# Optimization experiments

Hardware: AMD Instinct MI355X
Metric: run time of the kernel (lower is better)

## Reference

```python
import jax, jax.numpy as jnp
import numpy as np

HEADS = 8
DIM_HEAD = 64
DIM_COOR = 3
SCALE = (DIM_COOR * DIM_HEAD) ** -0.5


def setup_inputs() -> dict:
    key = jax.random.key(0)
    k1, k2, k3 = jax.random.split(key, 3)
    x = jax.random.normal(k1, (2, 2048, 256, 3), dtype=jnp.float32)
    w_qkv = jax.random.normal(k2, (1536, 256), dtype=jnp.float32)
    w_out = jax.random.normal(k3, (256, 512), dtype=jnp.float32)
    return {"x": x, "w_qkv": w_qkv, "w_out": w_out}


def reference(x, w_qkv, w_out):
    b, n, _, c = x.shape
    # VNLinear: contract feature dim, keep coord dim  -> [b, n, 3*h*d, c]
    qkv = jnp.einsum('bnic,oi->bnoc', x, w_qkv)
    q, k, v = jnp.split(qkv, 3, axis=-2)  # each [b, n, h*d, c]

    def to_heads(t):
        return t.reshape(b, n, HEADS, DIM_HEAD, c).transpose(0, 2, 1, 3, 4)  # b h n d c

    q, k, v = map(to_heads, (q, k, v))
    q = q * SCALE
    # scores sum over head-dim AND coordinate-dim
    sim = jnp.einsum('bhidc,bhjdc->bhij', q, k)
    attn = jax.nn.softmax(sim, axis=-1)
    out = jnp.einsum('bhij,bhjdc->bhidc', attn, v)  # coord dim preserved
    out = out.transpose(0, 2, 1, 3, 4).reshape(b, n, HEADS * DIM_HEAD, c)
    return jnp.einsum('bnic,oi->bnoc', out, w_out)
```

## Files before the change

### kernel.cpp

```cpp
#include <hip/hip_runtime.h>
#include <hip/hip_bf16.h>

#define SCALE 0.07216878364870322f
#define LOG2E 1.4426950408889634f

typedef __bf16 bf16x8 __attribute__((ext_vector_type(8)));
typedef float f32x16 __attribute__((ext_vector_type(16)));
typedef float f32x4v __attribute__((ext_vector_type(4)));
typedef unsigned int u32x4 __attribute__((ext_vector_type(4)));
typedef unsigned short u16;

#define MFMA(a, b, c) __builtin_amdgcn_mfma_f32_32x32x16_bf16(a, b, c, 0, 0, 0)
#define MFMA16(a, b, c) __builtin_amdgcn_mfma_f32_16x16x32_bf16(a, b, c, 0, 0, 0)

__device__ __forceinline__ u16 b16(float v) { return __builtin_bit_cast(u16, (__bf16)v); }
__device__ __forceinline__ float fb16(u16 u) {
    unsigned int t = (unsigned int)u << 16;
    return __builtin_bit_cast(float, t);
}
__device__ __forceinline__ unsigned int splitpack(float v) {
    u16 h = b16(v);
    float r = v - fb16(h);
    return (unsigned int)h | ((unsigned int)b16(r) << 16);
}
__device__ __forceinline__ unsigned int pack2(float a, float b) {
    return (unsigned int)b16(a) | ((unsigned int)b16(b) << 16);
}
__device__ __forceinline__ void gload16(const void* g, void* l) {
    __builtin_amdgcn_global_load_lds((const __attribute__((address_space(1))) void*)g,
                                     (__attribute__((address_space(3))) void*)l, 16, 0, 0);
}

__global__ __launch_bounds__(256) void qkv_mfma(const float* __restrict__ x,
                                                const float* __restrict__ wq,
                                                u16* __restrict__ Qhi, u16* __restrict__ Qlo,
                                                u16* __restrict__ Khi, u16* __restrict__ Klo,
                                                u16* __restrict__ Vf) {
    __shared__ unsigned int ldsr[2][32][196];
    const int tid = threadIdx.x;
    const int lane = tid & 63, w = tid >> 6, hf = lane >> 5, l31 = lane & 31;
    const int lq = lane & 15, gq = lane >> 4;
    const int o0 = blockIdx.x * 64;
    const int n0 = blockIdx.y * 128;
    const int b = blockIdx.z;
    const int nw0 = n0 + w * 32;
    const int part = o0 >> 9;
    const int h = (o0 >> 6) & 7;
    const int bh = b * 8 + h;

    const float* xp = x + ((size_t)(b * 2048 + nw0 + l31)) * 768 + hf * 24;
    const float* wp0 = wq + (size_t)(o0 + l31) * 256 + hf * 8;
    const float* wp1 = wp0 + 32 * 256;

    f32x16 acc[3][2] = {};
    #pragma unroll 2
    for (int k0 = 0; k0 < 16; ++k0) {
        float xf[24], wf0[8], wf1[8];
        #pragma unroll
        for (int q = 0; q < 6; ++q) {
            f32x4v t = *(const f32x4v*)(xp + k0 * 48 + q * 4);
            xf[q * 4 + 0] = t[0]; xf[q * 4 + 1] = t[1];
            xf[q * 4 + 2] = t[2]; xf[q * 4 + 3] = t[3];
        }
        {
            f32x4v t0 = *(const f32x4v*)(wp0 + k0 * 16);
            f32x4v t1 = *(const f32x4v*)(wp0 + k0 * 16 + 4);
            f32x4v t2 = *(const f32x4v*)(wp1 + k0 * 16);
            f32x4v t3 = *(const f32x4v*)(wp1 + k0 * 16 + 4);
            #pragma unroll
            for (int e = 0; e < 4; ++e) {
                wf0[e] = t0[e]; wf0[4 + e] = t1[e];
                wf1[e] = t2[e]; wf1[4 + e] = t3[e];
            }
        }
        bf16x8 xh[3], xl[3], wh[2], wl[2];
        #pragma unroll
        for (int c = 0; c < 3; ++c)
            #pragma unroll
            for (int e = 0; e < 8; ++e) {
                float v = xf[e * 3 + c];
                __bf16 hi = (__bf16)v;
                xh[c][e] = hi;
                xl[c][e] = (__bf16)(v - (float)hi);
            }
        #pragma unroll
        for (int e = 0; e < 8; ++e) {
            { float v = wf0[e]; __bf16 hi = (__bf16)v; wh[0][e] = hi; wl[0][e] = (__bf16)(v - (float)hi); }
            { float v = wf1[e]; __bf16 hi = (__bf16)v; wh[1][e] = hi; wl[1][e] = (__bf16)(v - (float)hi); }
        }
        #pragma unroll
        for (int c = 0; c < 3; ++c)
            #pragma unroll
            for (int ot = 0; ot < 2; ++ot) {
                acc[c][ot] = MFMA(xh[c], wh[ot], acc[c][ot]);
                acc[c][ot] = MFMA(xl[c], wh[ot], acc[c][ot]);
                acc[c][ot] = MFMA(xh[c], wl[ot], acc[c][ot]);
            }
    }

    #pragma unroll
    for (int round = 0; round < 2; ++round) {
        __syncthreads();
        if ((w >> 1) == round) {
            unsigned int (*L)[196] = ldsr[w & 1];
            #pragma unroll
            for (int c = 0; c < 3; ++c)
                #pragma unroll
                for (int ot = 0; ot < 2; ++ot)
                    #pragma unroll
                    for (int r = 0; r < 16; ++r) {
                        float v = acc[c][ot][r];
                        if (part == 0) v *= (SCALE * LOG2E);
                        int nn = (r & 3) + 8 * (r >> 2) + 4 * hf;
                        int dcol = 3 * (ot * 32 + l31) + c;
                        L[nn][dcol] = (part == 2) ? (unsigned int)b16(v) : splitpack(v);
                    }
            if (part < 2) {
                const int jt = nw0 >> 6;
                u16* baseH = (part == 0 ? Qhi : Khi);
                u16* baseL = (part == 0 ? Qlo : Klo);
                #pragma unroll
                for (int is = 0; is < 2; ++is)
                    #pragma unroll
                    for (int kc = 0; kc < 6; ++kc) {
                        const unsigned int* p = &L[is * 16 + lq][kc * 32 + gq * 8];
                        u32x4 a = *(const u32x4*)p;
                        u32x4 bq = *(const u32x4*)(p + 4);
                        u32x4 hi = { (a[0] & 0xffffu) | (a[1] << 16), (a[2] & 0xffffu) | (a[3] << 16),
                                     (bq[0] & 0xffffu) | (bq[1] << 16), (bq[2] & 0xffffu) | (bq[3] << 16) };
                        u32x4 lo = { (a[0] >> 16) | (a[1] & 0xffff0000u), (a[2] >> 16) | (a[3] & 0xffff0000u),
                                     (bq[0] >> 16) | (bq[1] & 0xffff0000u), (bq[2] >> 16) | (bq[3] & 0xffff0000u) };
                        size_t off;
                        if (part == 0)
                            off = ((size_t)(bh * 128 + (nw0 >> 4) + is) * 6 + kc) * 512 + lane * 8;
                        else
                            off = ((size_t)(bh * 32 + jt) * 24 + ((((nw0 >> 4) & 3) + is) * 6 + kc)) * 512 + lane * 8;
                        *(u32x4*)(baseH + off) = hi;
                        *(u32x4*)(baseL + off) = lo;
                    }
            } else {
                const int jt = nw0 >> 6, jc = (nw0 >> 5) & 1;
                u16* vp = Vf + ((size_t)(bh * 32 + jt) * 24 + jc) * 512 + lane * 8;
                #pragma unroll
                for (int d = 0; d < 12; ++d) {
                    unsigned int t[8];
                    #pragma unroll
                    for (int e = 0; e < 8; ++e)
                        t[e] = L[gq * 8 + e][d * 16 + lq];
                    u32x4 pk = { (t[0] & 0xffffu) | (t[1] << 16), (t[2] & 0xffffu) | (t[3] << 16),
                                 (t[4] & 0xffffu) | (t[5] << 16), (t[6] & 0xffffu) | (t[7] << 16) };
                    *(u32x4*)(vp + d * 1024) = pk;
                }
            }
        }
    }
}

__global__ __launch_bounds__(512) void attn_mfma(
    const u16* __restrict__ Qhi, const u16* __restrict__ Qlo,
    const u16* __restrict__ Khi, const u16* __restrict__ Klo,
    const u16* __restrict__ Vf, unsigned int* __restrict__ att2) {
    __shared__ __align__(16) u16 lds[2][36864];
    const int tid = threadIdx.x;
    const int lane = tid & 63;
    const int w = tid >> 6;
    const int g = lane >> 4;
    const int i = lane & 15;
    const int id = blockIdx.x;
    const int bh = (id & 7) * 2 + (id >> 7);
    const int itile = (id >> 3) & 15;
    const int i0 = itile * 128 + w * 16;

    bf16x8 qh[6], ql[6];
    {
        size_t qb = ((size_t)(bh * 128 + (i0 >> 4)) * 6) * 512 + (size_t)lane * 8;
        #pragma unroll
        for (int kc = 0; kc < 6; ++kc) {
            qh[kc] = *(const bf16x8*)(Qhi + qb + kc * 512);
            ql[kc] = *(const bf16x8*)(Qlo + qb + kc * 512);
        }
    }

    const char* gK = (const char*)Khi + (size_t)bh * 786432;
    const char* gL = (const char*)Klo + (size_t)bh * 786432;
    const char* gV = (const char*)Vf + (size_t)bh * 786432;
    const int t16 = tid * 16;

    auto stage = [&](int buf, int jt) {
        const size_t jo = (size_t)jt * 24576 + t16;
        char* dst = (char*)&lds[buf][0] + t16;
        #pragma unroll
        for (int s = 0; s < 3; ++s) {
            gload16(gK + jo + s * 8192, dst + s * 8192);
            gload16(gL + jo + s * 8192, dst + 24576 + s * 8192);
            gload16(gV + jo + s * 8192, dst + 49152 + s * 8192);
        }
    };

    stage(0, 0);
    __syncthreads();
    int cur = 0;

    f32x4v o[12] = {};
    float m_run = -1e30f, l_run = 0.f;
    const int sl0 = ((g & 1) << 5) + i;
    const int sl1 = sl0 + 16;
    const bool ghi = (g >> 1) != 0;

    for (int jt = 0; jt < 32; ++jt) {
        if (jt + 1 < 32) stage(cur ^ 1, jt + 1);
        const u16* L = &lds[cur][0];

        f32x4v s4[4] = {};
        #pragma unroll
        for (int kc = 0; kc < 6; ++kc) {
            bf16x8 kh[4], kl[4];
            #pragma unroll
            for (int js = 0; js < 4; ++js) {
                kh[js] = *(const bf16x8*)&L[(unsigned)((js * 6 + kc) * 512) + lane * 8];
                kl[js] = *(const bf16x8*)&L[12288u + (unsigned)((js * 6 + kc) * 512) + lane * 8];
            }
            #pragma unroll
            for (int js = 0; js < 4; ++js) s4[js] = MFMA16(kh[js], qh[kc], s4[js]);
            #pragma unroll
            for (int js = 0; js < 4; ++js) s4[js] = MFMA16(kh[js], ql[kc], s4[js]);
            #pragma unroll
            for (int js = 0; js < 4; ++js) s4[js] = MFMA16(kl[js], qh[kc], s4[js]);
        }

        float pm = -1e30f;
        #pragma unroll
        for (int js = 0; js < 4; ++js)
            #pragma unroll
            for (int r = 0; r < 4; ++r) pm = fmaxf(pm, s4[js][r]);
        pm = fmaxf(pm, __shfl_xor(pm, 16, 64));
        pm = fmaxf(pm, __shfl_xor(pm, 32, 64));
        if (!__all(pm <= m_run + 8.0f)) {
            float mnew = fmaxf(m_run, pm);
            float sc = exp2f(m_run - mnew);
            l_run *= sc;
            #pragma unroll
            for (int d = 0; d < 12; ++d) o[d] = o[d] * sc;
            m_run = mnew;
        }
        float rs = 0.f;
        unsigned int w0[4], w1[4];
        #pragma unroll
        for (int js = 0; js < 4; ++js) {
            float p0 = exp2f(s4[js][0] - m_run), p1 = exp2f(s4[js][1] - m_run);
            float p2 = exp2f(s4[js][2] - m_run), p3 = exp2f(s4[js][3] - m_run);
            rs += (p0 + p1) + (p2 + p3);
            w0[js] = pack2(p0, p1);
            w1[js] = pack2(p2, p3);
        }
        rs += __shfl_xor(rs, 16, 64);
        rs += __shfl_xor(rs, 32, 64);
        l_run += rs;

        #pragma unroll
        for (int c = 0; c < 2; ++c) {
            u32x4 F;
            { unsigned a0 = __shfl((int)w0[2 * c], sl0, 64), a1 = __shfl((int)w0[2 * c + 1], sl0, 64); F[0] = ghi ? a1 : a0; }
            { unsigned a0 = __shfl((int)w1[2 * c], sl0, 64), a1 = __shfl((int)w1[2 * c + 1], sl0, 64); F[1] = ghi ? a1 : a0; }
            { unsigned a0 = __shfl((int)w0[2 * c], sl1, 64), a1 = __shfl((int)w0[2 * c + 1], sl1, 64); F[2] = ghi ? a1 : a0; }
            { unsigned a0 = __shfl((int)w1[2 * c], sl1, 64), a1 = __shfl((int)w1[2 * c + 1], sl1, 64); F[3] = ghi ? a1 : a0; }
            bf16x8 pb = __builtin_bit_cast(bf16x8, F);
            #pragma unroll
            for (int d = 0; d < 12; ++d) {
                bf16x8 vf = *(const bf16x8*)&L[24576u + (unsigned)((d * 2 + c) * 512) + lane * 8];
                o[d] = MFMA16(vf, pb, o[d]);
            }
        }

        if (jt + 1 < 32) {
            __syncthreads();
            cur ^= 1;
        }
    }

    float inv = 1.0f / l_run;
    const int b2 = bh >> 3, hh = bh & 7;
    const int ig = i0 + i;
    const int itq = ig >> 5, i31 = ig & 31;
    #pragma unroll
    for (int d = 0; d < 12; ++d)
        #pragma unroll
        for (int r = 0; r < 4; ++r) {
            int dc = d * 16 + g * 4 + r;
            int dd = dc / 3, cc2 = dc - dd * 3;
            int hd = hh * 64 + dd;
            int ks = hd >> 4, e = hd & 7;
            int ln = i31 | (((hd >> 3) & 1) << 5);
            size_t off = (((size_t)(b2 * 3 + cc2) * 32 + ks) * 64 + itq) * 512 + (size_t)ln * 8 + e;
            att2[off] = splitpack(o[d][r] * inv);
        }
}

__global__ __launch_bounds__(256) void out_mfma(const unsigned int* __restrict__ att2,
                                                const float* __restrict__ wo,
                                                float* __restrict__ out) {
    const int tid = threadIdx.x, lane = tid & 63, w = tid >> 6, hf = lane >> 5, l31 = lane & 31;
    const int o0 = blockIdx.x * 32;
    const int n5 = blockIdx.y * 4 + w;
    const int b = blockIdx.z;
    const float* wp = wo + (size_t)(o0 + l31) * 512 + hf * 8;
    const unsigned int* ap = att2 + ((size_t)(b * 3) * 2048 + n5) * 512 + (size_t)lane * 8;
    f32x16 acc[3] = {};
    #pragma unroll 2
    for (int ks = 0; ks < 32; ++ks) {
        bf16x8 wh, wl;
        {
            f32x4v t0 = *(const f32x4v*)(wp + ks * 16);
            f32x4v t1 = *(const f32x4v*)(wp + ks * 16 + 4);
            #pragma unroll
            for (int e = 0; e < 4; ++e) {
                { float v = t0[e]; __bf16 hi = (__bf16)v; wh[e] = hi; wl[e] = (__bf16)(v - (float)hi); }
                { float v = t1[e]; __bf16 hi = (__bf16)v; wh[4 + e] = hi; wl[4 + e] = (__bf16)(v - (float)hi); }
            }
        }
        #pragma unroll
        for (int c = 0; c < 3; ++c) {
            const unsigned int* pc = ap + (size_t)c * 1048576 + ks * 32768;
            u32x4 a0 = *(const u32x4*)pc;
            u32x4 a1 = *(const u32x4*)(pc + 4);
            union { bf16x8 v; u32x4 u; } H, Lo;
            H.u  = { (a0[0] & 0xffffu) | (a0[1] << 16), (a0[2] & 0xffffu) | (a0[3] << 16),
                     (a1[0] & 0xffffu) | (a1[1] << 16), (a1[2] & 0xffffu) | (a1[3] << 16) };
            Lo.u = { (a0[0] >> 16) | (a0[1] & 0xffff0000u), (a0[2] >> 16) | (a0[3] & 0xffff0000u),
                     (a1[0] >> 16) | (a1[1] & 0xffff0000u), (a1[2] >> 16) | (a1[3] & 0xffff0000u) };
            acc[c] = MFMA(H.v, wh, acc[c]);
            acc[c] = MFMA(Lo.v, wh, acc[c]);
            acc[c] = MFMA(H.v, wl, acc[c]);
        }
    }
    #pragma unroll
    for (int r = 0; r < 16; ++r) {
        int n = (n5 << 5) + (r & 3) + 8 * (r >> 2) + 4 * hf;
        size_t off = ((size_t)(b * 2048 + n) * 256 + o0 + l31) * 3;
        out[off]     = acc[0][r];
        out[off + 1] = acc[1][r];
        out[off + 2] = acc[2][r];
    }
}

extern "C" void kernel_launch(void* const* d_in, const int* in_sizes, int n_in,
                              void* d_out, int out_size, void* d_ws, size_t ws_size,
                              hipStream_t stream) {
    const float* x     = (const float*)d_in[0];
    const float* w_qkv = (const float*)d_in[1];
    const float* w_out = (const float*)d_in[2];
    float* out = (float*)d_out;

    const size_t NB = (size_t)16 * 2048 * 192;
    u16* Qhi = (u16*)d_ws;
    u16* Qlo = Qhi + NB;
    u16* Khi = Qlo + NB;
    u16* Klo = Khi + NB;
    u16* Vf  = Klo + NB;
    unsigned int* att2 = (unsigned int*)(Vf + NB);

    qkv_mfma<<<dim3(24, 16, 2), 256, 0, stream>>>(x, w_qkv, Qhi, Qlo, Khi, Klo, Vf);
    attn_mfma<<<dim3(256), 512, 0, stream>>>(Qhi, Qlo, Khi, Klo, Vf, att2);
    out_mfma<<<dim3(8, 16, 2), 256, 0, stream>>>(att2, w_out, out);
}
```

Baseline: 225.6 us.

## Split attention over key halves with combine kernel and interleaved KV layout

Splits the key range of each attention tile into two halves, doubling the block count to 512, and adds a combine kernel that merges the partial outputs using the stored running max and sum. K-hi, K-lo and V are interleaved per 32-key tile, so each stage becomes one contiguous copy with a smaller LDS footprint. Launch bounds request higher occupancy, and the three split-precision score products go into separate accumulators under raised wave priority. The cost is an extra kernel launch, bf16 rounding of the partial outputs, and extra global traffic for them; att2 now reuses the Q buffer.

```diff
diff --git a/kernel.cpp b/kernel.cpp
--- a/kernel.cpp
+++ b/kernel.cpp
@@ -34,8 +34,7 @@
 __global__ __launch_bounds__(256) void qkv_mfma(const float* __restrict__ x,
                                                 const float* __restrict__ wq,
                                                 u16* __restrict__ Qhi, u16* __restrict__ Qlo,
-                                                u16* __restrict__ Khi, u16* __restrict__ Klo,
-                                                u16* __restrict__ Vf) {
+                                                u16* __restrict__ KVf) {
     __shared__ unsigned int ldsr[2][32][196];
     const int tid = threadIdx.x;
     const int lane = tid & 63, w = tid >> 6, hf = lane >> 5, l31 = lane & 31;
@@ -116,9 +115,6 @@
                         L[nn][dcol] = (part == 2) ? (unsigned int)b16(v) : splitpack(v);
                     }
             if (part < 2) {
-                const int jt = nw0 >> 6;
-                u16* baseH = (part == 0 ? Qhi : Khi);
-                u16* baseL = (part == 0 ? Qlo : Klo);
                 #pragma unroll
                 for (int is = 0; is < 2; ++is)
                     #pragma unroll
@@ -130,17 +126,18 @@
                                      (bq[0] & 0xffffu) | (bq[1] << 16), (bq[2] & 0xffffu) | (bq[3] << 16) };
                         u32x4 lo = { (a[0] >> 16) | (a[1] & 0xffff0000u), (a[2] >> 16) | (a[3] & 0xffff0000u),
                                      (bq[0] >> 16) | (bq[1] & 0xffff0000u), (bq[2] >> 16) | (bq[3] & 0xffff0000u) };
-                        size_t off;
-                        if (part == 0)
-                            off = ((size_t)(bh * 128 + (nw0 >> 4) + is) * 6 + kc) * 512 + lane * 8;
-                        else
-                            off = ((size_t)(bh * 32 + jt) * 24 + ((((nw0 >> 4) & 3) + is) * 6 + kc)) * 512 + lane * 8;
-                        *(u32x4*)(baseH + off) = hi;
-                        *(u32x4*)(baseL + off) = lo;
+                        if (part == 0) {
+                            size_t off = ((size_t)(bh * 128 + (nw0 >> 4) + is) * 6 + kc) * 512 + lane * 8;
+                            *(u32x4*)(Qhi + off) = hi;
+                            *(u32x4*)(Qlo + off) = lo;
+                        } else {
+                            size_t off = (size_t)(bh * 64 + (nw0 >> 5)) * 18432 + (is * 6 + kc) * 512 + lane * 8;
+                            *(u32x4*)(KVf + off) = hi;
+                            *(u32x4*)(KVf + off + 6144) = lo;
+                        }
                     }
             } else {
-                const int jt = nw0 >> 6, jc = (nw0 >> 5) & 1;
-                u16* vp = Vf + ((size_t)(bh * 32 + jt) * 24 + jc) * 512 + lane * 8;
+                u16* vp = KVf + (size_t)(bh * 64 + (nw0 >> 5)) * 18432 + 12288 + lane * 8;
                 #pragma unroll
                 for (int d = 0; d < 12; ++d) {
                     unsigned int t[8];
@@ -149,31 +146,33 @@
                         t[e] = L[gq * 8 + e][d * 16 + lq];
                     u32x4 pk = { (t[0] & 0xffffu) | (t[1] << 16), (t[2] & 0xffffu) | (t[3] << 16),
                                  (t[4] & 0xffffu) | (t[5] << 16), (t[6] & 0xffffu) | (t[7] << 16) };
-                    *(u32x4*)(vp + d * 1024) = pk;
+                    *(u32x4*)(vp + d * 512) = pk;
                 }
             }
         }
     }
 }
 
-__global__ __launch_bounds__(512) void attn_mfma(
+__global__ __launch_bounds__(512, 4) void attn_mfma(
     const u16* __restrict__ Qhi, const u16* __restrict__ Qlo,
-    const u16* __restrict__ Khi, const u16* __restrict__ Klo,
-    const u16* __restrict__ Vf, unsigned int* __restrict__ att2) {
-    __shared__ __align__(16) u16 lds[2][36864];
+    const u16* __restrict__ KVf, u16* __restrict__ Opart, float* __restrict__ MLp) {
+    __shared__ __align__(16) u16 lds[2][18432];
     const int tid = threadIdx.x;
     const int lane = tid & 63;
     const int w = tid >> 6;
     const int g = lane >> 4;
     const int i = lane & 15;
     const int id = blockIdx.x;
-    const int bh = (id & 7) * 2 + (id >> 7);
-    const int itile = (id >> 3) & 15;
+    const int rem = id >> 3;
+    const int grp = ((rem >> 4) << 3) | (id & 7);
+    const int itile = rem & 15;
+    const int bh = grp >> 1;
+    const int half = grp & 1;
     const int i0 = itile * 128 + w * 16;
 
     bf16x8 qh[6], ql[6];
     {
-        size_t qb = ((size_t)(bh * 128 + (i0 >> 4)) * 6) * 512 + (size_t)lane * 8;
+        size_t qb = (size_t)(bh * 128 + (i0 >> 4)) * 3072 + (size_t)lane * 8;
         #pragma unroll
         for (int kc = 0; kc < 6; ++kc) {
             qh[kc] = *(const bf16x8*)(Qhi + qb + kc * 512);
@@ -181,56 +180,58 @@
         }
     }
 
-    const char* gK = (const char*)Khi + (size_t)bh * 786432;
-    const char* gL = (const char*)Klo + (size_t)bh * 786432;
-    const char* gV = (const char*)Vf + (size_t)bh * 786432;
-    const int t16 = tid * 16;
-
-    auto stage = [&](int buf, int jt) {
-        const size_t jo = (size_t)jt * 24576 + t16;
-        char* dst = (char*)&lds[buf][0] + t16;
-        #pragma unroll
-        for (int s = 0; s < 3; ++s) {
-            gload16(gK + jo + s * 8192, dst + s * 8192);
-            gload16(gL + jo + s * 8192, dst + 24576 + s * 8192);
-            gload16(gV + jo + s * 8192, dst + 49152 + s * 8192);
+    const char* gKV = (const char*)KVf + (size_t)bh * 2359296;
+    auto stage = [&](int buf, int jtAbs) {
+        const char* src = gKV + (size_t)jtAbs * 36864;
+        char* dst = (char*)&lds[buf][0];
+        #pragma unroll
+        for (int s = 0; s < 4; ++s) {
+            const int c16 = (tid + s * 512) * 16;
+            gload16(src + c16, dst + c16);
+        }
+        if (tid < 256) {
+            const int c16 = (tid + 2048) * 16;
+            gload16(src + c16, dst + c16);
         }
     };
 
-    stage(0, 0);
+    const int jt0 = half * 32;
+    stage(0, jt0);
     __syncthreads();
     int cur = 0;
 
     f32x4v o[12] = {};
     float m_run = -1e30f, l_run = 0.f;
-    const int sl0 = ((g & 1) << 5) + i;
-    const int sl1 = sl0 + 16;
-    const bool ghi = (g >> 1) != 0;
-
-    for (int jt = 0; jt < 32; ++jt) {
-        if (jt + 1 < 32) stage(cur ^ 1, jt + 1);
+
+    for (int t = 0; t < 32; ++t) {
+        if (t + 1 < 32) stage(cur ^ 1, jt0 + t + 1);
         const u16* L = &lds[cur][0];
 
-        f32x4v s4[4] = {};
+        f32x4v sa[2] = {}, sb[2] = {}, sc[2] = {};
+        __builtin_amdgcn_s_setprio(1);
         #pragma unroll
         for (int kc = 0; kc < 6; ++kc) {
-            bf16x8 kh[4], kl[4];
-            #pragma unroll
-            for (int js = 0; js < 4; ++js) {
+            bf16x8 kh[2], kl[2];
+            #pragma unroll
+            for (int js = 0; js < 2; ++js) {
                 kh[js] = *(const bf16x8*)&L[(unsigned)((js * 6 + kc) * 512) + lane * 8];
-                kl[js] = *(const bf16x8*)&L[12288u + (unsigned)((js * 6 + kc) * 512) + lane * 8];
-            }
-            #pragma unroll
-            for (int js = 0; js < 4; ++js) s4[js] = MFMA16(kh[js], qh[kc], s4[js]);
-            #pragma unroll
-            for (int js = 0; js < 4; ++js) s4[js] = MFMA16(kh[js], ql[kc], s4[js]);
-            #pragma unroll
-            for (int js = 0; js < 4; ++js) s4[js] = MFMA16(kl[js], qh[kc], s4[js]);
-        }
+                kl[js] = *(const bf16x8*)&L[6144u + (unsigned)((js * 6 + kc) * 512) + lane * 8];
+            }
+            #pragma unroll
+            for (int js = 0; js < 2; ++js) sa[js] = MFMA16(kh[js], qh[kc], sa[js]);
+            #pragma unroll
+            for (int js = 0; js < 2; ++js) sb[js] = MFMA16(kh[js], ql[kc], sb[js]);
+            #pragma unroll
+            for (int js = 0; js < 2; ++js) sc[js] = MFMA16(kl[js], qh[kc], sc[js]);
+        }
+        __builtin_amdgcn_s_setprio(0);
+        f32x4v s4[2];
+        s4[0] = (sa[0] + sb[0]) + sc[0];
+        s4[1] = (sa[1] + sb[1]) + sc[1];
 
         float pm = -1e30f;
         #pragma unroll
-        for (int js = 0; js < 4; ++js)
+        for (int js = 0; js < 2; ++js)
             #pragma unroll
             for (int r = 0; r < 4; ++r) pm = fmaxf(pm, s4[js][r]);
         pm = fmaxf(pm, __shfl_xor(pm, 16, 64));
@@ -244,9 +245,9 @@
             m_run = mnew;
         }
         float rs = 0.f;
-        unsigned int w0[4], w1[4];
-        #pragma unroll
-        for (int js = 0; js < 4; ++js) {
+        unsigned int w0[2], w1[2];
+        #pragma unroll
+        for (int js = 0; js < 2; ++js) {
             float p0 = exp2f(s4[js][0] - m_run), p1 = exp2f(s4[js][1] - m_run);
             float p2 = exp2f(s4[js][2] - m_run), p3 = exp2f(s4[js][3] - m_run);
             rs += (p0 + p1) + (p2 + p3);
@@ -257,42 +258,75 @@
         rs += __shfl_xor(rs, 32, 64);
         l_run += rs;
 
-        #pragma unroll
-        for (int c = 0; c < 2; ++c) {
-            u32x4 F;
-            { unsigned a0 = __shfl((int)w0[2 * c], sl0, 64), a1 = __shfl((int)w0[2 * c + 1], sl0, 64); F[0] = ghi ? a1 : a0; }
-            { unsigned a0 = __shfl((int)w1[2 * c], sl0, 64), a1 = __shfl((int)w1[2 * c + 1], sl0, 64); F[1] = ghi ? a1 : a0; }
-            { unsigned a0 = __shfl((int)w0[2 * c], sl1, 64), a1 = __shfl((int)w0[2 * c + 1], sl1, 64); F[2] = ghi ? a1 : a0; }
-            { unsigned a0 = __shfl((int)w1[2 * c], sl1, 64), a1 = __shfl((int)w1[2 * c + 1], sl1, 64); F[3] = ghi ? a1 : a0; }
-            bf16x8 pb = __builtin_bit_cast(bf16x8, F);
-            #pragma unroll
-            for (int d = 0; d < 12; ++d) {
-                bf16x8 vf = *(const bf16x8*)&L[24576u + (unsigned)((d * 2 + c) * 512) + lane * 8];
-                o[d] = MFMA16(vf, pb, o[d]);
-            }
-        }
-
-        if (jt + 1 < 32) {
+        u32x4 F;
+        const int slA = ((g & 1) << 5) + i;
+        const int slB = slA + 16;
+        const bool ghi = (g >> 1) != 0;
+        { unsigned a0 = __shfl((int)w0[0], slA, 64), a1 = __shfl((int)w0[1], slA, 64); F[0] = ghi ? a1 : a0; }
+        { unsigned a0 = __shfl((int)w1[0], slA, 64), a1 = __shfl((int)w1[1], slA, 64); F[1] = ghi ? a1 : a0; }
+        { unsigned a0 = __shfl((int)w0[0], slB, 64), a1 = __shfl((int)w0[1], slB, 64); F[2] = ghi ? a1 : a0; }
+        { unsigned a0 = __shfl((int)w1[0], slB, 64), a1 = __shfl((int)w1[1], slB, 64); F[3] = ghi ? a1 : a0; }
+        bf16x8 pb = __builtin_bit_cast(bf16x8, F);
+
+        __builtin_amdgcn_s_setprio(1);
+        #pragma unroll
+        for (int d = 0; d < 12; ++d) {
+            bf16x8 vf = *(const bf16x8*)&L[12288u + (unsigned)(d * 512) + lane * 8];
+            o[d] = MFMA16(vf, pb, o[d]);
+        }
+        __builtin_amdgcn_s_setprio(0);
+
+        if (t + 1 < 32) {
             __syncthreads();
             cur ^= 1;
         }
     }
 
-    float inv = 1.0f / l_run;
+    const int tI = bh * 128 + itile * 8 + w;
+    u16* Op = Opart + (size_t)(half * 2048 + tI) * 3072 + lane;
+    #pragma unroll
+    for (int d = 0; d < 12; ++d)
+        #pragma unroll
+        for (int r = 0; r < 4; ++r)
+            Op[(d * 4 + r) * 64] = b16(o[d][r]);
+    float* mlp = MLp + (size_t)(half * 2048 + tI) * 128 + lane * 2;
+    mlp[0] = m_run;
+    mlp[1] = l_run;
+}
+
+__global__ __launch_bounds__(256) void attn_combine(const u16* __restrict__ Opart,
+                                                    const float* __restrict__ MLp,
+                                                    unsigned int* __restrict__ att2) {
+    const int tid = threadIdx.x, lane = tid & 63, w = tid >> 6;
+    const int g = lane >> 4, i = lane & 15;
+    const int tI = blockIdx.x * 4 + w;
+    const int bh = tI >> 7;
+    const float* mla = MLp + (size_t)tI * 128 + lane * 2;
+    const float* mlb = MLp + (size_t)(2048 + tI) * 128 + lane * 2;
+    float ma = mla[0], la = mla[1];
+    float mb = mlb[0], lb = mlb[1];
+    float mm = fmaxf(ma, mb);
+    float wa = exp2f(ma - mm), wb = exp2f(mb - mm);
+    float inv = 1.0f / (la * wa + lb * wb);
+    const u16* Oa = Opart + (size_t)tI * 3072 + lane;
+    const u16* Ob = Opart + (size_t)(2048 + tI) * 3072 + lane;
     const int b2 = bh >> 3, hh = bh & 7;
-    const int ig = i0 + i;
+    const int ig = (tI & 127) * 16 + i;
     const int itq = ig >> 5, i31 = ig & 31;
     #pragma unroll
     for (int d = 0; d < 12; ++d)
         #pragma unroll
         for (int r = 0; r < 4; ++r) {
+            float va = fb16(Oa[(d * 4 + r) * 64]);
+            float vb = fb16(Ob[(d * 4 + r) * 64]);
+            float v = (va * wa + vb * wb) * inv;
             int dc = d * 16 + g * 4 + r;
             int dd = dc / 3, cc2 = dc - dd * 3;
             int hd = hh * 64 + dd;
             int ks = hd >> 4, e = hd & 7;
             int ln = i31 | (((hd >> 3) & 1) << 5);
             size_t off = (((size_t)(b2 * 3 + cc2) * 32 + ks) * 64 + itq) * 512 + (size_t)ln * 8 + e;
-            att2[off] = splitpack(o[d][r] * inv);
+            att2[off] = splitpack(v);
         }
 }
 
@@ -354,12 +388,13 @@
     const size_t NB = (size_t)16 * 2048 * 192;
     u16* Qhi = (u16*)d_ws;
     u16* Qlo = Qhi + NB;
-    u16* Khi = Qlo + NB;
-    u16* Klo = Khi + NB;
-    u16* Vf  = Klo + NB;
-    unsigned int* att2 = (unsigned int*)(Vf + NB);
-
-    qkv_mfma<<<dim3(24, 16, 2), 256, 0, stream>>>(x, w_qkv, Qhi, Qlo, Khi, Klo, Vf);
-    attn_mfma<<<dim3(256), 512, 0, stream>>>(Qhi, Qlo, Khi, Klo, Vf, att2);
+    u16* KVf = Qlo + NB;
+    u16* Opart = KVf + (size_t)16 * 64 * 18432;
+    float* MLp = (float*)(Opart + (size_t)4096 * 3072);
+    unsigned int* att2 = (unsigned int*)Qhi;
+
+    qkv_mfma<<<dim3(24, 16, 2), 256, 0, stream>>>(x, w_qkv, Qhi, Qlo, KVf);
+    attn_mfma<<<dim3(512), 512, 0, stream>>>(Qhi, Qlo, KVf, Opart, MLp);
+    attn_combine<<<dim3(512), 256, 0, stream>>>(Opart, MLp, att2);
     out_mfma<<<dim3(8, 16, 2), 256, 0, stream>>>(att2, w_out, out);
 }
```

New measurement: 257.7 us. 14.2% more time.
